# Performance work log

Measured on AMD Instinct MI355X. Metric: run time of the kernel, lower is better.

Reference implementation:

```python
import jax, jax.numpy as jnp
import numpy as np

B, T, IN, H = 256, 512, 64, 256
G = 4 * H  # gates i,f,g,o (PyTorch order)


def setup_inputs() -> dict:
    key = jax.random.key(0)
    ks = jax.random.split(key, 9)
    s_in = 1.0 / np.sqrt(H)
    return {
        "x": jax.random.normal(ks[0], (B, T, IN), jnp.float32),
        "Wih0": jax.random.normal(ks[1], (2, G, IN), jnp.float32) * s_in,
        "Whh0": jax.random.normal(ks[2], (2, G, H), jnp.float32) * s_in,
        "b0": jax.random.normal(ks[3], (2, G), jnp.float32) * s_in,
        "Wih1": jax.random.normal(ks[4], (2, G, 2 * H), jnp.float32) * s_in,
        "Whh1": jax.random.normal(ks[5], (2, G, H), jnp.float32) * s_in,
        "b1": jax.random.normal(ks[6], (2, G), jnp.float32) * s_in,
        "fc_w": jax.random.normal(ks[7], (1, 2 * H), jnp.float32) * s_in,
        "fc_b": jnp.zeros((1,), jnp.float32),
    }


def _lstm_dir(x, Wih, Whh, b, reverse):
    """One direction of one LSTM layer. x: [B,T,F] -> hs: [B,T,H]."""
    Bb = x.shape[0]
    Hh = Whh.shape[1]
    if reverse:
        x = jnp.flip(x, axis=1)
    # precompute input contribution for all timesteps (one big GEMM)
    xg = jnp.einsum('btf,gf->btg', x, Wih) + b  # [B,T,4H]

    def step(carry, g_t):
        h, c = carry
        g = g_t + h @ Whh.T  # [B,4H]
        i, f, gg, o = jnp.split(g, 4, axis=-1)
        i = jax.nn.sigmoid(i)
        f = jax.nn.sigmoid(f)
        gg = jnp.tanh(gg)
        o = jax.nn.sigmoid(o)
        c = f * c + i * gg
        h = o * jnp.tanh(c)
        return (h, c), h

    h0 = jnp.zeros((Bb, Hh), x.dtype)
    (_, _), hs = jax.lax.scan(step, (h0, h0), jnp.swapaxes(xg, 0, 1))
    hs = jnp.swapaxes(hs, 0, 1)  # [B,T,H]
    if reverse:
        hs = jnp.flip(hs, axis=1)
    return hs


def _bilstm_layer(x, Wih, Whh, b):
    hf = _lstm_dir(x, Wih[0], Whh[0], b[0], False)
    hb = _lstm_dir(x, Wih[1], Whh[1], b[1], True)
    return jnp.concatenate([hf, hb], axis=-1)  # [B,T,2H]


def reference(x, Wih0, Whh0, b0, Wih1, Whh1, b1, fc_w, fc_b):
    h = _bilstm_layer(x, Wih0, Whh0, b0)
    # inter-layer dropout: identity (eval mode)
    h = _bilstm_layer(h, Wih1, Whh1, b1)
    last = h[:, -1, :]  # [B,2H]
    # final dropout: identity (eval mode)
    return last @ fc_w.T + fc_b  # [B,1]
```

## Files before the change

### kernel.cpp

```cpp
#include <hip/hip_runtime.h>


#define T_ 512
#define IN_ 64
#define H_ 256

typedef __attribute__((ext_vector_type(8))) _Float16 f16x8;
typedef __attribute__((ext_vector_type(4))) _Float16 f16x4;
typedef __attribute__((ext_vector_type(4))) float f32x4;
typedef unsigned long long u64;
typedef unsigned int u32;

__device__ __forceinline__ float sigm(float x){ return 1.f/(1.f+__expf(-x)); }
__device__ __forceinline__ float tanh_(float x){ return 1.f - 2.f/(__expf(2.f*x)+1.f); }

__global__ void pack_w(const float* __restrict__ ih, const float* __restrict__ hh,
                       _Float16* __restrict__ dst, int KX, int KH, int KT,
                       int QW, int NSUB, int NQ, int total) {
    int idx = blockIdx.x * 256 + threadIdx.x;
    if (idx >= total) return;
    int e = idx & 7, lane = (idx >> 3) & 63;
    int u = idx >> 9;
    int kt = u % KT; u /= KT;
    int sub = u % NSUB; u /= NSUB;
    int gt = u & 3; u >>= 2;
    int q = u % NQ; int dir = u / NQ;
    int g = gt * 256 + q * QW + sub * 16 + (lane & 15);
    int k = kt * 32 + (lane >> 4) * 8 + e;
    float v = (k < KX) ? ih[(size_t)(dir * 1024 + g) * KX + k]
                       : hh[(size_t)(dir * 1024 + g) * KH + (k - KX)];
    dst[idx] = (_Float16)v;
}

template <int KXT, int KHT, int QW, bool IS_L0>
__global__ __launch_bounds__(256)
void lstm_scan(const float* __restrict__ x, const _Float16* __restrict__ xin,
               const _Float16* __restrict__ wpack, const float* __restrict__ bias,
               u64* __restrict__ hbuf,
               _Float16* __restrict__ out0, float* __restrict__ hlast) {
    constexpr int MROWS = 16;
    constexpr int KT = KXT + KHT, KX = KXT * 32;
    constexpr int NTHR = 256;
    constexpr int NSUB = QW / 16, NQ = 256 / QW;
    constexpr int NGRP = IS_L0 ? 32 : 16;
    constexpr int WBE = 4 * NSUB * KT * 512;
    constexpr int KP = KX + 8;
    constexpr int HPW = 132;
    constexpr int GP = QW + 1;
    constexpr int NWORD = MROWS * 128;
    constexpr int NW = NWORD / NTHR;
    constexpr int OWNW = QW / 2;

    extern __shared__ char smem[];
    _Float16* w_lds = (_Float16*)smem;
    u32*      h32   = (u32*)(smem + (size_t)WBE * 2);
    _Float16* a_lds = (_Float16*)(smem + (size_t)WBE * 2 + (size_t)MROWS * HPW * 4);
    float*    g_lds = (float*)(smem + (size_t)WBE * 2 + (size_t)MROWS * HPW * 4
                               + (size_t)MROWS * KP * 2);

    const int tid = threadIdx.x, lane = tid & 63, wave = tid >> 6;
    const int grp = blockIdx.x % NGRP, q = blockIdx.x / NGRP;
    const int dir = IS_L0 ? (grp >> 4) : 0;
    const int b0r = (IS_L0 ? (grp & 15) : grp) * MROWS;
    const int gt = wave;

    {
        const f16x8* src = (const f16x8*)(wpack + (size_t)(dir * NQ + q) * WBE);
        f16x8* dst = (f16x8*)w_lds;
        for (int i = tid; i < WBE / 8; i += NTHR) dst[i] = src[i];
    }

    const int erow = tid >> 4, ecp = tid & 15;
    float b_[4][NSUB], c_reg[NSUB];
#pragma unroll
    for (int g4 = 0; g4 < 4; ++g4)
#pragma unroll
        for (int j = 0; j < NSUB; ++j)
            b_[g4][j] = bias[dir * 1024 + g4 * 256 + q * QW + ecp * NSUB + j];
#pragma unroll
    for (int j = 0; j < NSUB; ++j) c_reg[j] = 0.f;

    const int colp = tid & 127;
    const bool skip = (colp >= q * OWNW) && (colp < q * OWNW + OWNW);

    float4 xv;
    f16x8 xp[4];
    {
        int t0 = dir ? (T_ - 1) : 0;
        int t1 = dir ? (T_ - 2) : 1;
        if constexpr (IS_L0) {
            const int xrow = tid >> 4, c4 = (tid & 15) * 4;
            float4 v0 = *(const float4*)&x[((size_t)(b0r + xrow) * T_ + t0) * IN_ + c4];
            f16x4 h4; h4[0]=(_Float16)v0.x; h4[1]=(_Float16)v0.y; h4[2]=(_Float16)v0.z; h4[3]=(_Float16)v0.w;
            *(f16x4*)&a_lds[(size_t)xrow * KP + c4] = h4;
            xv = *(const float4*)&x[((size_t)(b0r + xrow) * T_ + t1) * IN_ + c4];
        } else {
#pragma unroll
            for (int j = 0; j < 4; ++j) {
                int ch = j * NTHR + tid;
                int r2 = ch >> 6, c8 = (ch & 63) * 8;
                f16x8 v = *(const f16x8*)&xin[((size_t)(b0r + r2) * T_ + t0) * 512 + c8];
                *(f16x8*)&a_lds[(size_t)r2 * KP + c8] = v;
            }
#pragma unroll
            for (int j = 0; j < 4; ++j) {
                int ch = j * NTHR + tid;
                int r2 = ch >> 6, c8 = (ch & 63) * 8;
                xp[j] = *(const f16x8*)&xin[((size_t)(b0r + r2) * T_ + t1) * 512 + c8];
            }
        }
    }
    __syncthreads();

    const int arow = lane & 15;
    const int kc8 = (lane >> 4) * 8;

    for (int s = 0; s < T_; ++s) {
        const int t = dir ? (T_ - 1 - s) : s;

        f32x4 acc[NSUB][2];
#pragma unroll
        for (int sub = 0; sub < NSUB; ++sub) {
            f32x4 z = {0.f, 0.f, 0.f, 0.f};
            acc[sub][0] = z; acc[sub][1] = z;
        }
#pragma unroll
        for (int kt = 0; kt < KXT; ++kt) {
            f16x8 a = *(const f16x8*)&a_lds[(size_t)arow * KP + kt * 32 + kc8];
#pragma unroll
            for (int sub = 0; sub < NSUB; ++sub) {
                f16x8 b = *(const f16x8*)&w_lds[(((size_t)(gt * NSUB + sub) * KT + kt) * 64 + lane) * 8];
                acc[sub][kt & 1] = __builtin_amdgcn_mfma_f32_16x16x32_f16(a, b, acc[sub][kt & 1], 0, 0, 0);
            }
        }

        if (s > 0 && !skip) {
            const u32 want = (u32)(s - 1);
            u64* bw = hbuf + ((size_t)grp * 2 + ((s - 1) & 1)) * NWORD;
            u64 ga[NW];
            u32 pend = (1u << NW) - 1u;
#pragma unroll
            for (int k = 0; k < NW; ++k)
                ga[k] = __hip_atomic_load(&bw[k * NTHR + tid], __ATOMIC_RELAXED,
                                          __HIP_MEMORY_SCOPE_AGENT);
            for (;;) {
#pragma unroll
                for (int k = 0; k < NW; ++k) {
                    if ((pend & (1u << k)) && (u32)(ga[k] >> 32) == want) {
                        int w = k * NTHR + tid;
                        h32[(size_t)(w >> 7) * HPW + (w & 127)] = (u32)ga[k];
                        pend &= ~(1u << k);
                    }
                }
                if (!pend) break;
#pragma unroll
                for (int k = 0; k < NW; ++k)
                    if (pend & (1u << k))
                        ga[k] = __hip_atomic_load(&bw[k * NTHR + tid], __ATOMIC_RELAXED,
                                                  __HIP_MEMORY_SCOPE_AGENT);
            }
        }
        __syncthreads();

        if constexpr (IS_L0) {
            const int xrow = tid >> 4, c4 = (tid & 15) * 4;
            f16x4 h4; h4[0]=(_Float16)xv.x; h4[1]=(_Float16)xv.y; h4[2]=(_Float16)xv.z; h4[3]=(_Float16)xv.w;
            *(f16x4*)&a_lds[(size_t)xrow * KP + c4] = h4;
        } else {
#pragma unroll
            for (int j = 0; j < 4; ++j) {
                int ch = j * NTHR + tid;
                int r2 = ch >> 6, c8 = (ch & 63) * 8;
                *(f16x8*)&a_lds[(size_t)r2 * KP + c8] = xp[j];
            }
        }

        if (s > 0) {
#pragma unroll
            for (int kt = 0; kt < KHT; ++kt) {
                f16x8 a = *(const f16x8*)&h32[(size_t)arow * HPW + kt * 16 + (lane >> 4) * 4];
#pragma unroll
                for (int sub = 0; sub < NSUB; ++sub) {
                    f16x8 b = *(const f16x8*)&w_lds[(((size_t)(gt * NSUB + sub) * KT + KXT + kt) * 64 + lane) * 8];
                    acc[sub][kt & 1] = __builtin_amdgcn_mfma_f32_16x16x32_f16(a, b, acc[sub][kt & 1], 0, 0, 0);
                }
            }
        }
        {
            const int crow = (lane >> 4) * 4, ccol = lane & 15;
#pragma unroll
            for (int sub = 0; sub < NSUB; ++sub) {
                f32x4 av = acc[sub][0] + acc[sub][1];
#pragma unroll
                for (int qq = 0; qq < 4; ++qq)
                    g_lds[(size_t)(gt * MROWS + crow + qq) * GP + sub * 16 + ccol] = av[qq];
            }
        }
        __syncthreads();

        float hval[NSUB];
#pragma unroll
        for (int j = 0; j < NSUB; ++j) {
            float gI = g_lds[(size_t)(0 * MROWS + erow) * GP + ecp * NSUB + j] + b_[0][j];
            float gF = g_lds[(size_t)(1 * MROWS + erow) * GP + ecp * NSUB + j] + b_[1][j];
            float gG = g_lds[(size_t)(2 * MROWS + erow) * GP + ecp * NSUB + j] + b_[2][j];
            float gO = g_lds[(size_t)(3 * MROWS + erow) * GP + ecp * NSUB + j] + b_[3][j];
            float i_ = sigm(gI), f_ = sigm(gF), g2 = tanh_(gG), o_ = sigm(gO);
            c_reg[j] = f_ * c_reg[j] + i_ * g2;
            hval[j] = o_ * tanh_(c_reg[j]);
        }
        {
            u64* bw = hbuf + ((size_t)grp * 2 + (s & 1)) * NWORD;
            if constexpr (NSUB == 2) {
                union { _Float16 h[2]; u32 u; } pk;
                pk.h[0] = (_Float16)hval[0]; pk.h[1] = (_Float16)hval[1];
                if (s + 1 < T_) {
                    u64 word = (u64)pk.u | ((u64)(u32)s << 32);
                    __hip_atomic_store(&bw[erow * 128 + q * 16 + ecp], word,
                                       __ATOMIC_RELAXED, __HIP_MEMORY_SCOPE_AGENT);
                    h32[(size_t)erow * HPW + q * 16 + ecp] = pk.u;
                }
                if constexpr (IS_L0) {
                    *(u32*)&out0[((size_t)(b0r + erow) * T_ + t) * 512 + dir * 256 + q * QW + ecp * 2] = pk.u;
                }
            } else {
                union { _Float16 h; unsigned short u; } hb; hb.h = (_Float16)hval[0];
                u32 ov = (u32)__shfl_xor((int)hb.u, 1);
                u32 lo = (u32)hb.u | ((ov & 0xFFFFu) << 16);
                if (!(lane & 1) && s + 1 < T_) {
                    u64 word = (u64)lo | ((u64)(u32)s << 32);
                    __hip_atomic_store(&bw[erow * 128 + ((q * 16 + ecp) >> 1)], word,
                                       __ATOMIC_RELAXED, __HIP_MEMORY_SCOPE_AGENT);
                    h32[(size_t)erow * HPW + q * (QW / 2) + (ecp >> 1)] = lo;
                }
            }
        }

        if constexpr (!IS_L0) {
            if (s == T_ - 1)
                hlast[(size_t)(b0r + erow) * 256 + q * QW + ecp] = hval[0];
        }
        {
            int sn2 = (s + 2 < T_) ? s + 2 : T_ - 1;
            int t2 = dir ? (T_ - 1 - sn2) : sn2;
            if constexpr (IS_L0) {
                const int xrow = tid >> 4, c4 = (tid & 15) * 4;
                xv = *(const float4*)&x[((size_t)(b0r + xrow) * T_ + t2) * IN_ + c4];
            } else {
#pragma unroll
                for (int j = 0; j < 4; ++j) {
                    int ch = j * NTHR + tid;
                    int r2 = ch >> 6, c8 = (ch & 63) * 8;
                    xp[j] = *(const f16x8*)&xin[((size_t)(b0r + r2) * T_ + t2) * 512 + c8];
                }
            }
        }
    }
}

__global__ __launch_bounds__(256)
void tail_kernel(const _Float16* __restrict__ out0, const float* __restrict__ Wih1,
                 const float* __restrict__ b1, const float* __restrict__ fcw,
                 const float* __restrict__ fcb, const float* __restrict__ h1f,
                 float* __restrict__ out) {
    const int b = blockIdx.x, tid = threadIdx.x;
    __shared__ float xs[512];
    __shared__ float red[256];
    for (int i = tid; i < 512; i += 256)
        xs[i] = (float)out0[((size_t)b * T_ + (T_ - 1)) * 512 + i];
    __syncthreads();
    const float* Wb = Wih1 + (size_t)1024 * 512;
    const float* wI = Wb + (size_t)tid * 512;
    const float* wG = Wb + (size_t)(512 + tid) * 512;
    const float* wO = Wb + (size_t)(768 + tid) * 512;
    float aI = 0.f, aG = 0.f, aO = 0.f;
    for (int k = 0; k < 512; k += 4) {
        float4 xv = *(const float4*)&xs[k];
        float4 w0 = *(const float4*)&wI[k];
        float4 w1 = *(const float4*)&wG[k];
        float4 w2 = *(const float4*)&wO[k];
        aI += xv.x * w0.x + xv.y * w0.y + xv.z * w0.z + xv.w * w0.w;
        aG += xv.x * w1.x + xv.y * w1.y + xv.z * w1.z + xv.w * w1.w;
        aO += xv.x * w2.x + xv.y * w2.y + xv.z * w2.z + xv.w * w2.w;
    }
    float i_ = sigm(aI + b1[1024 + tid]);
    float g_ = tanh_(aG + b1[1024 + 512 + tid]);
    float o_ = sigm(aO + b1[1024 + 768 + tid]);
    float c = i_ * g_;
    float hb = o_ * tanh_(c);
    float part = h1f[b * 256 + tid] * fcw[tid] + hb * fcw[256 + tid];
    red[tid] = part;
    __syncthreads();
    for (int sx = 128; sx > 0; sx >>= 1) {
        if (tid < sx) red[tid] += red[tid + sx];
        __syncthreads();
    }
    if (tid == 0) out[b] = red[0] + fcb[0];
}

extern "C" void kernel_launch(void* const* d_in, const int* in_sizes, int n_in,
                              void* d_out, int out_size, void* d_ws, size_t ws_size,
                              hipStream_t stream) {
    const float* x    = (const float*)d_in[0];
    const float* Wih0 = (const float*)d_in[1];
    const float* Whh0 = (const float*)d_in[2];
    const float* b0   = (const float*)d_in[3];
    const float* Wih1 = (const float*)d_in[4];
    const float* Whh1 = (const float*)d_in[5];
    const float* b1   = (const float*)d_in[6];
    const float* fcw  = (const float*)d_in[7];
    const float* fcb  = (const float*)d_in[8];

    char* ws = (char*)d_ws;
    _Float16* W0pack = (_Float16*)(ws + 0);
    _Float16* W1pack = (_Float16*)(ws + 1310720);
    u64* hbuf0       = (u64*)(ws + 2883584);
    u64* hbuf1       = (u64*)(ws + 3932160);
    float* h1f       = (float*)(ws + 4456448);
    _Float16* out0   = (_Float16*)(ws + 4718592);

    hipMemsetAsync(ws + 2883584, 0xFF, 1572864, stream);

    hipLaunchKernelGGL(pack_w, dim3(2560), dim3(256), 0, stream,
                       Wih0, Whh0, W0pack, 64, 256, 10, 32, 2, 8, 655360);
    hipLaunchKernelGGL(pack_w, dim3(3072), dim3(256), 0, stream,
                       Wih1, Whh1, W1pack, 512, 256, 24, 16, 1, 16, 786432);

    hipFuncSetAttribute((const void*)(lstm_scan<2, 8, 32, true>),
                        hipFuncAttributeMaxDynamicSharedMemorySize, 101120);
    hipFuncSetAttribute((const void*)(lstm_scan<16, 8, 16, false>),
                        hipFuncAttributeMaxDynamicSharedMemorySize, 127744);

    hipLaunchKernelGGL((lstm_scan<2, 8, 32, true>), dim3(256), dim3(256), 101120, stream,
                       x, (const _Float16*)nullptr, W0pack, b0, hbuf0,
                       out0, (float*)nullptr);
    hipLaunchKernelGGL((lstm_scan<16, 8, 16, false>), dim3(256), dim3(256), 127744, stream,
                       (const float*)nullptr, (const _Float16*)out0, W1pack, b1, hbuf1,
                       (_Float16*)nullptr, h1f);
    hipLaunchKernelGGL(tail_kernel, dim3(256), dim3(256), 0, stream,
                       out0, Wih1, b1, fcw, fcb, h1f, (float*)d_out);
}
```

Measured before the change: 2.304 ms.

## Interleave two batch groups per block to hide cross-block h exchange latency

Each block now handles two 16-row batch groups in alternation, halving the grid to 128 blocks and doubling the h, activation and gate buffers in LDS. While one group waits on the global h exchange, the other group's MFMA work and gate math can run, and the polling loads for the next step are issued right after storing the current h so they overlap the other group's compute. This costs more LDS and registers per block, extra __syncthreads per step, and serial work per block, with only half as many blocks working in parallel.

```diff
diff --git a/kernel.cpp b/kernel.cpp
--- a/kernel.cpp
+++ b/kernel.cpp
@@ -42,7 +42,7 @@
     constexpr int KT = KXT + KHT, KX = KXT * 32;
     constexpr int NTHR = 256;
     constexpr int NSUB = QW / 16, NQ = 256 / QW;
-    constexpr int NGRP = IS_L0 ? 32 : 16;
+    constexpr int NPAIR = IS_L0 ? 16 : 8;
     constexpr int WBE = 4 * NSUB * KT * 512;
     constexpr int KP = KX + 8;
     constexpr int HPW = 132;
@@ -54,14 +54,16 @@
     extern __shared__ char smem[];
     _Float16* w_lds = (_Float16*)smem;
     u32*      h32   = (u32*)(smem + (size_t)WBE * 2);
-    _Float16* a_lds = (_Float16*)(smem + (size_t)WBE * 2 + (size_t)MROWS * HPW * 4);
-    float*    g_lds = (float*)(smem + (size_t)WBE * 2 + (size_t)MROWS * HPW * 4
-                               + (size_t)MROWS * KP * 2);
+    _Float16* a_all = (_Float16*)(smem + (size_t)WBE * 2 + 2u * MROWS * HPW * 4);
+    float*    g_all = (float*)(smem + (size_t)WBE * 2 + 2u * MROWS * HPW * 4
+                               + 2u * MROWS * KP * 2);
 
     const int tid = threadIdx.x, lane = tid & 63, wave = tid >> 6;
-    const int grp = blockIdx.x % NGRP, q = blockIdx.x / NGRP;
-    const int dir = IS_L0 ? (grp >> 4) : 0;
-    const int b0r = (IS_L0 ? (grp & 15) : grp) * MROWS;
+    const int p = blockIdx.x % NPAIR, q = blockIdx.x / NPAIR;
+    const int dir = IS_L0 ? (p >> 3) : 0;
+    const int bgp = IS_L0 ? (p & 7) : p;
+    const int grp0 = dir * 16 + bgp * 2;
+    const int b0rbase = bgp * 32;
     const int gt = wave;
 
     {
@@ -71,42 +73,50 @@
     }
 
     const int erow = tid >> 4, ecp = tid & 15;
-    float b_[4][NSUB], c_reg[NSUB];
+    float b_[4][NSUB];
 #pragma unroll
     for (int g4 = 0; g4 < 4; ++g4)
 #pragma unroll
         for (int j = 0; j < NSUB; ++j)
             b_[g4][j] = bias[dir * 1024 + g4 * 256 + q * QW + ecp * NSUB + j];
-#pragma unroll
-    for (int j = 0; j < NSUB; ++j) c_reg[j] = 0.f;
+    float c_reg[2][NSUB];
+#pragma unroll
+    for (int g01 = 0; g01 < 2; ++g01)
+#pragma unroll
+        for (int j = 0; j < NSUB; ++j) c_reg[g01][j] = 0.f;
 
     const int colp = tid & 127;
     const bool skip = (colp >= q * OWNW) && (colp < q * OWNW + OWNW);
 
-    float4 xv;
-    f16x8 xp[4];
+    float4 xv[2];
+    f16x8 xp[2][4];
     {
         int t0 = dir ? (T_ - 1) : 0;
         int t1 = dir ? (T_ - 2) : 1;
-        if constexpr (IS_L0) {
-            const int xrow = tid >> 4, c4 = (tid & 15) * 4;
-            float4 v0 = *(const float4*)&x[((size_t)(b0r + xrow) * T_ + t0) * IN_ + c4];
-            f16x4 h4; h4[0]=(_Float16)v0.x; h4[1]=(_Float16)v0.y; h4[2]=(_Float16)v0.z; h4[3]=(_Float16)v0.w;
-            *(f16x4*)&a_lds[(size_t)xrow * KP + c4] = h4;
-            xv = *(const float4*)&x[((size_t)(b0r + xrow) * T_ + t1) * IN_ + c4];
-        } else {
-#pragma unroll
-            for (int j = 0; j < 4; ++j) {
-                int ch = j * NTHR + tid;
-                int r2 = ch >> 6, c8 = (ch & 63) * 8;
-                f16x8 v = *(const f16x8*)&xin[((size_t)(b0r + r2) * T_ + t0) * 512 + c8];
-                *(f16x8*)&a_lds[(size_t)r2 * KP + c8] = v;
-            }
-#pragma unroll
-            for (int j = 0; j < 4; ++j) {
-                int ch = j * NTHR + tid;
-                int r2 = ch >> 6, c8 = (ch & 63) * 8;
-                xp[j] = *(const f16x8*)&xin[((size_t)(b0r + r2) * T_ + t1) * 512 + c8];
+#pragma unroll
+        for (int g01 = 0; g01 < 2; ++g01) {
+            _Float16* a_g = a_all + (size_t)g01 * MROWS * KP;
+            const int b0r = b0rbase + g01 * 16;
+            if constexpr (IS_L0) {
+                const int xrow = tid >> 4, c4 = (tid & 15) * 4;
+                float4 v0 = *(const float4*)&x[((size_t)(b0r + xrow) * T_ + t0) * IN_ + c4];
+                f16x4 h4; h4[0]=(_Float16)v0.x; h4[1]=(_Float16)v0.y; h4[2]=(_Float16)v0.z; h4[3]=(_Float16)v0.w;
+                *(f16x4*)&a_g[(size_t)xrow * KP + c4] = h4;
+                xv[g01] = *(const float4*)&x[((size_t)(b0r + xrow) * T_ + t1) * IN_ + c4];
+            } else {
+#pragma unroll
+                for (int j = 0; j < 4; ++j) {
+                    int ch = j * NTHR + tid;
+                    int r2 = ch >> 6, c8 = (ch & 63) * 8;
+                    f16x8 v = *(const f16x8*)&xin[((size_t)(b0r + r2) * T_ + t0) * 512 + c8];
+                    *(f16x8*)&a_g[(size_t)r2 * KP + c8] = v;
+                }
+#pragma unroll
+                for (int j = 0; j < 4; ++j) {
+                    int ch = j * NTHR + tid;
+                    int r2 = ch >> 6, c8 = (ch & 63) * 8;
+                    xp[g01][j] = *(const f16x8*)&xin[((size_t)(b0r + r2) * T_ + t1) * 512 + c8];
+                }
             }
         }
     }
@@ -115,110 +125,115 @@
     const int arow = lane & 15;
     const int kc8 = (lane >> 4) * 8;
 
+    u64 ga[2][NW];
+
     for (int s = 0; s < T_; ++s) {
         const int t = dir ? (T_ - 1 - s) : s;
 
-        f32x4 acc[NSUB][2];
-#pragma unroll
-        for (int sub = 0; sub < NSUB; ++sub) {
-            f32x4 z = {0.f, 0.f, 0.f, 0.f};
-            acc[sub][0] = z; acc[sub][1] = z;
-        }
-#pragma unroll
-        for (int kt = 0; kt < KXT; ++kt) {
-            f16x8 a = *(const f16x8*)&a_lds[(size_t)arow * KP + kt * 32 + kc8];
+#pragma unroll
+        for (int g01 = 0; g01 < 2; ++g01) {
+            _Float16* a_g = a_all + (size_t)g01 * MROWS * KP;
+            u32* h32g = h32 + (size_t)g01 * MROWS * HPW;
+            float* g_g = g_all + (size_t)g01 * 4 * MROWS * GP;
+            const int grp = grp0 + g01;
+            const int b0r = b0rbase + g01 * 16;
+
+            f32x4 acc[NSUB][2];
 #pragma unroll
             for (int sub = 0; sub < NSUB; ++sub) {
-                f16x8 b = *(const f16x8*)&w_lds[(((size_t)(gt * NSUB + sub) * KT + kt) * 64 + lane) * 8];
-                acc[sub][kt & 1] = __builtin_amdgcn_mfma_f32_16x16x32_f16(a, b, acc[sub][kt & 1], 0, 0, 0);
-            }
-        }
-
-        if (s > 0 && !skip) {
-            const u32 want = (u32)(s - 1);
-            u64* bw = hbuf + ((size_t)grp * 2 + ((s - 1) & 1)) * NWORD;
-            u64 ga[NW];
-            u32 pend = (1u << NW) - 1u;
-#pragma unroll
-            for (int k = 0; k < NW; ++k)
-                ga[k] = __hip_atomic_load(&bw[k * NTHR + tid], __ATOMIC_RELAXED,
-                                          __HIP_MEMORY_SCOPE_AGENT);
-            for (;;) {
-#pragma unroll
-                for (int k = 0; k < NW; ++k) {
-                    if ((pend & (1u << k)) && (u32)(ga[k] >> 32) == want) {
-                        int w = k * NTHR + tid;
-                        h32[(size_t)(w >> 7) * HPW + (w & 127)] = (u32)ga[k];
-                        pend &= ~(1u << k);
+                f32x4 z = {0.f, 0.f, 0.f, 0.f};
+                acc[sub][0] = z; acc[sub][1] = z;
+            }
+#pragma unroll
+            for (int kt = 0; kt < KXT; ++kt) {
+                f16x8 a = *(const f16x8*)&a_g[(size_t)arow * KP + kt * 32 + kc8];
+#pragma unroll
+                for (int sub = 0; sub < NSUB; ++sub) {
+                    f16x8 b = *(const f16x8*)&w_lds[(((size_t)(gt * NSUB + sub) * KT + kt) * 64 + lane) * 8];
+                    acc[sub][kt & 1] = __builtin_amdgcn_mfma_f32_16x16x32_f16(a, b, acc[sub][kt & 1], 0, 0, 0);
+                }
+            }
+
+            if (s > 0 && !skip) {
+                const u32 want = (u32)(s - 1);
+                u64* bw = hbuf + ((size_t)grp * 2 + ((s - 1) & 1)) * NWORD;
+                u32 pend = (1u << NW) - 1u;
+                for (;;) {
+#pragma unroll
+                    for (int k = 0; k < NW; ++k) {
+                        if ((pend & (1u << k)) && (u32)(ga[g01][k] >> 32) == want) {
+                            int w = k * NTHR + tid;
+                            h32g[(size_t)(w >> 7) * HPW + (w & 127)] = (u32)ga[g01][k];
+                            pend &= ~(1u << k);
+                        }
                     }
-                }
-                if (!pend) break;
-#pragma unroll
-                for (int k = 0; k < NW; ++k)
-                    if (pend & (1u << k))
-                        ga[k] = __hip_atomic_load(&bw[k * NTHR + tid], __ATOMIC_RELAXED,
-                                                  __HIP_MEMORY_SCOPE_AGENT);
-            }
-        }
-        __syncthreads();
-
-        if constexpr (IS_L0) {
-            const int xrow = tid >> 4, c4 = (tid & 15) * 4;
-            f16x4 h4; h4[0]=(_Float16)xv.x; h4[1]=(_Float16)xv.y; h4[2]=(_Float16)xv.z; h4[3]=(_Float16)xv.w;
-            *(f16x4*)&a_lds[(size_t)xrow * KP + c4] = h4;
-        } else {
-#pragma unroll
-            for (int j = 0; j < 4; ++j) {
-                int ch = j * NTHR + tid;
-                int r2 = ch >> 6, c8 = (ch & 63) * 8;
-                *(f16x8*)&a_lds[(size_t)r2 * KP + c8] = xp[j];
-            }
-        }
-
-        if (s > 0) {
-#pragma unroll
-            for (int kt = 0; kt < KHT; ++kt) {
-                f16x8 a = *(const f16x8*)&h32[(size_t)arow * HPW + kt * 16 + (lane >> 4) * 4];
+                    if (!pend) break;
+#pragma unroll
+                    for (int k = 0; k < NW; ++k)
+                        if (pend & (1u << k))
+                            ga[g01][k] = __hip_atomic_load(&bw[k * NTHR + tid], __ATOMIC_RELAXED,
+                                                           __HIP_MEMORY_SCOPE_AGENT);
+                }
+            }
+            __syncthreads();
+
+            if constexpr (IS_L0) {
+                const int xrow = tid >> 4, c4 = (tid & 15) * 4;
+                f16x4 h4; h4[0]=(_Float16)xv[g01].x; h4[1]=(_Float16)xv[g01].y;
+                h4[2]=(_Float16)xv[g01].z; h4[3]=(_Float16)xv[g01].w;
+                *(f16x4*)&a_g[(size_t)xrow * KP + c4] = h4;
+            } else {
+#pragma unroll
+                for (int j = 0; j < 4; ++j) {
+                    int ch = j * NTHR + tid;
+                    int r2 = ch >> 6, c8 = (ch & 63) * 8;
+                    *(f16x8*)&a_g[(size_t)r2 * KP + c8] = xp[g01][j];
+                }
+            }
+
+            if (s > 0) {
+#pragma unroll
+                for (int kt = 0; kt < KHT; ++kt) {
+                    f16x8 a = *(const f16x8*)&h32g[(size_t)arow * HPW + kt * 16 + (lane >> 4) * 4];
+#pragma unroll
+                    for (int sub = 0; sub < NSUB; ++sub) {
+                        f16x8 b = *(const f16x8*)&w_lds[(((size_t)(gt * NSUB + sub) * KT + KXT + kt) * 64 + lane) * 8];
+                        acc[sub][kt & 1] = __builtin_amdgcn_mfma_f32_16x16x32_f16(a, b, acc[sub][kt & 1], 0, 0, 0);
+                    }
+                }
+            }
+            {
+                const int crow = (lane >> 4) * 4, ccol = lane & 15;
 #pragma unroll
                 for (int sub = 0; sub < NSUB; ++sub) {
-                    f16x8 b = *(const f16x8*)&w_lds[(((size_t)(gt * NSUB + sub) * KT + KXT + kt) * 64 + lane) * 8];
-                    acc[sub][kt & 1] = __builtin_amdgcn_mfma_f32_16x16x32_f16(a, b, acc[sub][kt & 1], 0, 0, 0);
-                }
-            }
-        }
-        {
-            const int crow = (lane >> 4) * 4, ccol = lane & 15;
-#pragma unroll
-            for (int sub = 0; sub < NSUB; ++sub) {
-                f32x4 av = acc[sub][0] + acc[sub][1];
-#pragma unroll
-                for (int qq = 0; qq < 4; ++qq)
-                    g_lds[(size_t)(gt * MROWS + crow + qq) * GP + sub * 16 + ccol] = av[qq];
-            }
-        }
-        __syncthreads();
-
-        float hval[NSUB];
-#pragma unroll
-        for (int j = 0; j < NSUB; ++j) {
-            float gI = g_lds[(size_t)(0 * MROWS + erow) * GP + ecp * NSUB + j] + b_[0][j];
-            float gF = g_lds[(size_t)(1 * MROWS + erow) * GP + ecp * NSUB + j] + b_[1][j];
-            float gG = g_lds[(size_t)(2 * MROWS + erow) * GP + ecp * NSUB + j] + b_[2][j];
-            float gO = g_lds[(size_t)(3 * MROWS + erow) * GP + ecp * NSUB + j] + b_[3][j];
-            float i_ = sigm(gI), f_ = sigm(gF), g2 = tanh_(gG), o_ = sigm(gO);
-            c_reg[j] = f_ * c_reg[j] + i_ * g2;
-            hval[j] = o_ * tanh_(c_reg[j]);
-        }
-        {
-            u64* bw = hbuf + ((size_t)grp * 2 + (s & 1)) * NWORD;
+                    f32x4 av = acc[sub][0] + acc[sub][1];
+#pragma unroll
+                    for (int qq = 0; qq < 4; ++qq)
+                        g_g[(size_t)(gt * MROWS + crow + qq) * GP + sub * 16 + ccol] = av[qq];
+                }
+            }
+            __syncthreads();
+
+            float hval[NSUB];
+#pragma unroll
+            for (int j = 0; j < NSUB; ++j) {
+                float gI = g_g[(size_t)(0 * MROWS + erow) * GP + ecp * NSUB + j] + b_[0][j];
+                float gF = g_g[(size_t)(1 * MROWS + erow) * GP + ecp * NSUB + j] + b_[1][j];
+                float gG = g_g[(size_t)(2 * MROWS + erow) * GP + ecp * NSUB + j] + b_[2][j];
+                float gO = g_g[(size_t)(3 * MROWS + erow) * GP + ecp * NSUB + j] + b_[3][j];
+                float i_ = sigm(gI), f_ = sigm(gF), g2 = tanh_(gG), o_ = sigm(gO);
+                c_reg[g01][j] = f_ * c_reg[g01][j] + i_ * g2;
+                hval[j] = o_ * tanh_(c_reg[g01][j]);
+            }
+            u64* bw2 = hbuf + ((size_t)grp * 2 + (s & 1)) * NWORD;
             if constexpr (NSUB == 2) {
                 union { _Float16 h[2]; u32 u; } pk;
                 pk.h[0] = (_Float16)hval[0]; pk.h[1] = (_Float16)hval[1];
                 if (s + 1 < T_) {
                     u64 word = (u64)pk.u | ((u64)(u32)s << 32);
-                    __hip_atomic_store(&bw[erow * 128 + q * 16 + ecp], word,
+                    __hip_atomic_store(&bw2[erow * 128 + q * 16 + ecp], word,
                                        __ATOMIC_RELAXED, __HIP_MEMORY_SCOPE_AGENT);
-                    h32[(size_t)erow * HPW + q * 16 + ecp] = pk.u;
+                    h32g[(size_t)erow * HPW + q * 16 + ecp] = pk.u;
                 }
                 if constexpr (IS_L0) {
                     *(u32*)&out0[((size_t)(b0r + erow) * T_ + t) * 512 + dir * 256 + q * QW + ecp * 2] = pk.u;
@@ -229,30 +244,35 @@
                 u32 lo = (u32)hb.u | ((ov & 0xFFFFu) << 16);
                 if (!(lane & 1) && s + 1 < T_) {
                     u64 word = (u64)lo | ((u64)(u32)s << 32);
-                    __hip_atomic_store(&bw[erow * 128 + ((q * 16 + ecp) >> 1)], word,
+                    __hip_atomic_store(&bw2[erow * 128 + ((q * 16 + ecp) >> 1)], word,
                                        __ATOMIC_RELAXED, __HIP_MEMORY_SCOPE_AGENT);
-                    h32[(size_t)erow * HPW + q * (QW / 2) + (ecp >> 1)] = lo;
-                }
-            }
-        }
-
-        if constexpr (!IS_L0) {
-            if (s == T_ - 1)
-                hlast[(size_t)(b0r + erow) * 256 + q * QW + ecp] = hval[0];
-        }
-        {
-            int sn2 = (s + 2 < T_) ? s + 2 : T_ - 1;
-            int t2 = dir ? (T_ - 1 - sn2) : sn2;
-            if constexpr (IS_L0) {
-                const int xrow = tid >> 4, c4 = (tid & 15) * 4;
-                xv = *(const float4*)&x[((size_t)(b0r + xrow) * T_ + t2) * IN_ + c4];
-            } else {
-#pragma unroll
-                for (int j = 0; j < 4; ++j) {
-                    int ch = j * NTHR + tid;
-                    int r2 = ch >> 6, c8 = (ch & 63) * 8;
-                    xp[j] = *(const f16x8*)&xin[((size_t)(b0r + r2) * T_ + t2) * 512 + c8];
-                }
+                    h32g[(size_t)erow * HPW + q * (QW / 2) + (ecp >> 1)] = lo;
+                }
+            }
+            if constexpr (!IS_L0) {
+                if (s == T_ - 1)
+                    hlast[(size_t)(b0r + erow) * 256 + q * QW + ecp] = hval[0];
+            }
+            {
+                int sn2 = (s + 2 < T_) ? s + 2 : T_ - 1;
+                int t2 = dir ? (T_ - 1 - sn2) : sn2;
+                if constexpr (IS_L0) {
+                    const int xrow = tid >> 4, c4 = (tid & 15) * 4;
+                    xv[g01] = *(const float4*)&x[((size_t)(b0r + xrow) * T_ + t2) * IN_ + c4];
+                } else {
+#pragma unroll
+                    for (int j = 0; j < 4; ++j) {
+                        int ch = j * NTHR + tid;
+                        int r2 = ch >> 6, c8 = (ch & 63) * 8;
+                        xp[g01][j] = *(const f16x8*)&xin[((size_t)(b0r + r2) * T_ + t2) * 512 + c8];
+                    }
+                }
+            }
+            if (s + 1 < T_ && !skip) {
+#pragma unroll
+                for (int k = 0; k < NW; ++k)
+                    ga[g01][k] = __hip_atomic_load(&bw2[k * NTHR + tid], __ATOMIC_RELAXED,
+                                                   __HIP_MEMORY_SCOPE_AGENT);
             }
         }
     }
@@ -327,14 +347,14 @@
                        Wih1, Whh1, W1pack, 512, 256, 24, 16, 1, 16, 786432);
 
     hipFuncSetAttribute((const void*)(lstm_scan<2, 8, 32, true>),
-                        hipFuncAttributeMaxDynamicSharedMemorySize, 101120);
+                        hipFuncAttributeMaxDynamicSharedMemorySize, 120320);
     hipFuncSetAttribute((const void*)(lstm_scan<16, 8, 16, false>),
-                        hipFuncAttributeMaxDynamicSharedMemorySize, 127744);
-
-    hipLaunchKernelGGL((lstm_scan<2, 8, 32, true>), dim3(256), dim3(256), 101120, stream,
+                        hipFuncAttributeMaxDynamicSharedMemorySize, 157184);
+
+    hipLaunchKernelGGL((lstm_scan<2, 8, 32, true>), dim3(128), dim3(256), 120320, stream,
                        x, (const _Float16*)nullptr, W0pack, b0, hbuf0,
                        out0, (float*)nullptr);
-    hipLaunchKernelGGL((lstm_scan<16, 8, 16, false>), dim3(256), dim3(256), 127744, stream,
+    hipLaunchKernelGGL((lstm_scan<16, 8, 16, false>), dim3(128), dim3(256), 157184, stream,
                        (const float*)nullptr, (const _Float16*)out0, W1pack, b1, hbuf1,
                        (_Float16*)nullptr, h1f);
     hipLaunchKernelGGL(tail_kernel, dim3(256), dim3(256), 0, stream,
```

Result: slower. 5.708 ms (+147.7%).

## Widen layer-0 column slices to 64 and keep input weights in registers

Applied to the files above, without the earlier changes.

Layer 0 now splits each direction's gate columns across 4 blocks of 64 columns instead of 8 blocks of 32, halving the layer-0 grid to 128 blocks and the number of peers that exchange hidden-state chunks each step. To fit the larger weight slice in LDS, the small input-projection weights are held in registers and only the recurrent weights are staged in LDS. A new NSUB==4 path packs and publishes four hidden values per thread. This cuts cross-block synchronisation traffic per step, at the cost of more MFMA work per block, higher register pressure and fewer active CUs.

```diff
diff --git a/kernel.cpp b/kernel.cpp
--- a/kernel.cpp
+++ b/kernel.cpp
@@ -43,6 +43,7 @@
     constexpr int NTHR = 256;
     constexpr int NSUB = QW / 16, NQ = 256 / QW;
     constexpr int NGRP = IS_L0 ? 32 : 16;
+    constexpr bool XREG = IS_L0;
     constexpr int WBE = 4 * NSUB * KT * 512;
     constexpr int KP = KX + 8;
     constexpr int HPW = 132;
@@ -53,9 +54,10 @@
 
     extern __shared__ char smem[];
     _Float16* w_lds = (_Float16*)smem;
-    u32*      h32   = (u32*)(smem + (size_t)WBE * 2);
-    _Float16* a_lds = (_Float16*)(smem + (size_t)WBE * 2 + (size_t)MROWS * HPW * 4);
-    float*    g_lds = (float*)(smem + (size_t)WBE * 2 + (size_t)MROWS * HPW * 4
+    constexpr int WLDS = XREG ? (4 * NSUB * KHT * 512) : WBE;
+    u32*      h32   = (u32*)(smem + (size_t)WLDS * 2);
+    _Float16* a_lds = (_Float16*)(smem + (size_t)WLDS * 2 + (size_t)MROWS * HPW * 4);
+    float*    g_lds = (float*)(smem + (size_t)WLDS * 2 + (size_t)MROWS * HPW * 4
                                + (size_t)MROWS * KP * 2);
 
     const int tid = threadIdx.x, lane = tid & 63, wave = tid >> 6;
@@ -64,10 +66,29 @@
     const int b0r = (IS_L0 ? (grp & 15) : grp) * MROWS;
     const int gt = wave;
 
+    const f16x8* wsrc8 = (const f16x8*)(wpack + (size_t)(dir * NQ + q) * WBE);
+
+    f16x8 bx[NSUB][KXT > 0 ? KXT : 1];
+    if constexpr (XREG) {
+#pragma unroll
+        for (int sub = 0; sub < NSUB; ++sub)
+#pragma unroll
+            for (int kt = 0; kt < KXT; ++kt)
+                bx[sub][kt] = wsrc8[(size_t)((gt * NSUB + sub) * KT + kt) * 64 + lane];
+    }
+
     {
-        const f16x8* src = (const f16x8*)(wpack + (size_t)(dir * NQ + q) * WBE);
-        f16x8* dst = (f16x8*)w_lds;
-        for (int i = tid; i < WBE / 8; i += NTHR) dst[i] = src[i];
+        f16x8* wdst = (f16x8*)w_lds;
+        if constexpr (XREG) {
+            for (int i = tid; i < WLDS / 8; i += NTHR) {
+                int sidx = i >> 9;
+                int rem = i & 511;
+                int kth = rem >> 6, l = rem & 63;
+                wdst[i] = wsrc8[(size_t)(sidx * KT + KXT + kth) * 64 + l];
+            }
+        } else {
+            for (int i = tid; i < WLDS / 8; i += NTHR) wdst[i] = wsrc8[i];
+        }
     }
 
     const int erow = tid >> 4, ecp = tid & 15;
@@ -129,7 +150,9 @@
             f16x8 a = *(const f16x8*)&a_lds[(size_t)arow * KP + kt * 32 + kc8];
 #pragma unroll
             for (int sub = 0; sub < NSUB; ++sub) {
-                f16x8 b = *(const f16x8*)&w_lds[(((size_t)(gt * NSUB + sub) * KT + kt) * 64 + lane) * 8];
+                f16x8 b;
+                if constexpr (XREG) b = bx[sub][kt];
+                else b = *(const f16x8*)&w_lds[(((size_t)(gt * NSUB + sub) * KT + kt) * 64 + lane) * 8];
                 acc[sub][kt & 1] = __builtin_amdgcn_mfma_f32_16x16x32_f16(a, b, acc[sub][kt & 1], 0, 0, 0);
             }
         }
@@ -181,7 +204,11 @@
                 f16x8 a = *(const f16x8*)&h32[(size_t)arow * HPW + kt * 16 + (lane >> 4) * 4];
 #pragma unroll
                 for (int sub = 0; sub < NSUB; ++sub) {
-                    f16x8 b = *(const f16x8*)&w_lds[(((size_t)(gt * NSUB + sub) * KT + KXT + kt) * 64 + lane) * 8];
+                    f16x8 b;
+                    if constexpr (XREG)
+                        b = *(const f16x8*)&w_lds[(((size_t)(gt * NSUB + sub) * KHT + kt) * 64 + lane) * 8];
+                    else
+                        b = *(const f16x8*)&w_lds[(((size_t)(gt * NSUB + sub) * KT + KXT + kt) * 64 + lane) * 8];
                     acc[sub][kt & 1] = __builtin_amdgcn_mfma_f32_16x16x32_f16(a, b, acc[sub][kt & 1], 0, 0, 0);
                 }
             }
@@ -211,7 +238,25 @@
         }
         {
             u64* bw = hbuf + ((size_t)grp * 2 + (s & 1)) * NWORD;
-            if constexpr (NSUB == 2) {
+            if constexpr (NSUB == 4) {
+                union { _Float16 h[2]; u32 u; } pk0, pk1;
+                pk0.h[0] = (_Float16)hval[0]; pk0.h[1] = (_Float16)hval[1];
+                pk1.h[0] = (_Float16)hval[2]; pk1.h[1] = (_Float16)hval[3];
+                const int wcol = q * 32 + ecp * 2;
+                if (s + 1 < T_) {
+                    u64 tg = ((u64)(u32)s << 32);
+                    __hip_atomic_store(&bw[erow * 128 + wcol], (u64)pk0.u | tg,
+                                       __ATOMIC_RELAXED, __HIP_MEMORY_SCOPE_AGENT);
+                    __hip_atomic_store(&bw[erow * 128 + wcol + 1], (u64)pk1.u | tg,
+                                       __ATOMIC_RELAXED, __HIP_MEMORY_SCOPE_AGENT);
+                    h32[(size_t)erow * HPW + wcol] = pk0.u;
+                    h32[(size_t)erow * HPW + wcol + 1] = pk1.u;
+                }
+                if constexpr (IS_L0) {
+                    u64 ov = (u64)pk0.u | ((u64)pk1.u << 32);
+                    *(u64*)&out0[((size_t)(b0r + erow) * T_ + t) * 512 + dir * 256 + q * QW + ecp * 4] = ov;
+                }
+            } else if constexpr (NSUB == 2) {
                 union { _Float16 h[2]; u32 u; } pk;
                 pk.h[0] = (_Float16)hval[0]; pk.h[1] = (_Float16)hval[1];
                 if (s + 1 < T_) {
@@ -322,16 +367,16 @@
     hipMemsetAsync(ws + 2883584, 0xFF, 1572864, stream);
 
     hipLaunchKernelGGL(pack_w, dim3(2560), dim3(256), 0, stream,
-                       Wih0, Whh0, W0pack, 64, 256, 10, 32, 2, 8, 655360);
+                       Wih0, Whh0, W0pack, 64, 256, 10, 64, 4, 4, 655360);
     hipLaunchKernelGGL(pack_w, dim3(3072), dim3(256), 0, stream,
                        Wih1, Whh1, W1pack, 512, 256, 24, 16, 1, 16, 786432);
 
-    hipFuncSetAttribute((const void*)(lstm_scan<2, 8, 32, true>),
-                        hipFuncAttributeMaxDynamicSharedMemorySize, 101120);
+    hipFuncSetAttribute((const void*)(lstm_scan<2, 8, 64, true>),
+                        hipFuncAttributeMaxDynamicSharedMemorySize, 158464);
     hipFuncSetAttribute((const void*)(lstm_scan<16, 8, 16, false>),
                         hipFuncAttributeMaxDynamicSharedMemorySize, 127744);
 
-    hipLaunchKernelGGL((lstm_scan<2, 8, 32, true>), dim3(256), dim3(256), 101120, stream,
+    hipLaunchKernelGGL((lstm_scan<2, 8, 64, true>), dim3(128), dim3(256), 158464, stream,
                        x, (const _Float16*)nullptr, W0pack, b0, hbuf0,
                        out0, (float*)nullptr);
     hipLaunchKernelGGL((lstm_scan<16, 8, 16, false>), dim3(256), dim3(256), 127744, stream,
```

New measurement: 2.477 ms. 1.07x slower.
